# Kernel optimization log

Hardware: AMD Instinct MI355X
Metric: run time of the kernel (lower is better)

## Reference

```python
import jax, jax.numpy as jnp
import numpy as np

ITER_STEPS = 2


def setup_inputs() -> dict:
    key = jax.random.key(0)
    ks = jax.random.split(key, 9)
    B, N, D, E = 64, 256, 512, 10  # batch, nodes, node_dim, edge types
    node = jax.random.normal(ks[0], (B, N, D), dtype=jnp.float32)
    node_mask = jax.random.randint(ks[1], (B, N), 0, 2).astype(jnp.int32)
    adj = jax.random.randint(ks[2], (E, B, N, N), 0, 2).astype(jnp.int32)
    s = 0.02
    W_nw = jax.random.normal(ks[3], (1, D), dtype=jnp.float32) * s   # node weight fc [out=1, in=D]
    b_nw = jnp.zeros((1,), dtype=jnp.float32)
    W_self = jax.random.normal(ks[4], (D, D), dtype=jnp.float32) * s
    b_self = jnp.zeros((D,), dtype=jnp.float32)
    W_edge = jax.random.normal(ks[5], (E, D, D), dtype=jnp.float32) * s  # per-edge-type Linear (no bias)
    return {"node": node, "W_nw": W_nw, "b_nw": b_nw, "W_self": W_self,
            "b_self": b_self, "W_edge": W_edge, "node_mask": node_mask, "adj": adj}


def reference(node, W_nw, b_nw, W_self, b_self, W_edge, node_mask, adj):
    # node: [B,N,D]; node_mask: [B,N] int; adj: [E=10,B,N,N] int (binary)
    B, N, D = node.shape
    m = node_mask.astype(node.dtype)
    eye = jnp.eye(N, dtype=node.dtype)
    # dd_graph = mask outer-product with zeroed diagonal: [B,N,N]
    dd = m[:, None, :] * m[:, :, None] * (1.0 - eye)
    graphs = dd[None] * adj.astype(node.dtype)  # [E,B,N,N]
    # total neighbor count across all 10 edge types, clamped to >=1 (replace_masked_values)
    neigh = graphs.sum(axis=(0, 3))                       # [B,N]
    neigh = jnp.where(neigh >= 1.0, neigh, 1.0)
    all_weight = []
    for _ in range(ITER_STEPS):
        # (1) node relatedness gate
        w = jax.nn.sigmoid(node @ W_nw.T + b_nw)[..., 0]  # [B,N]
        all_weight.append(w)
        self_info = node @ W_self.T + b_self              # [B,N,D]
        # (2) per-edge-type projection + masked adjacency matmul, summed over edge types
        proj = jnp.einsum('bnk,edk->ebnd', node, W_edge)  # [E,B,N,D]
        masked_w = jnp.where(graphs != 0, w[None, :, None, :], 0.0)  # [E,B,N,N]
        agg = jnp.einsum('ebnm,ebmd->bnd', masked_w, proj)           # [B,N,D]
        # (3) update
        node = jax.nn.relu(self_info + agg / neigh[..., None])
    return node, jnp.stack(all_weight, axis=1)  # ([B,N,D], [B,ITER,N])
```

## Files before the change

kernel.cpp:

```cpp
#include <hip/hip_runtime.h>
#include <hip/hip_bf16.h>

#define BB 64
#define NN 256
#define DD 512
#define EE 10

typedef __bf16 bf16x8 __attribute__((ext_vector_type(8)));
typedef unsigned short ushort8v __attribute__((ext_vector_type(8)));
typedef unsigned int uint4v __attribute__((ext_vector_type(4)));
typedef unsigned int uint2v __attribute__((ext_vector_type(2)));
typedef float floatx4 __attribute__((ext_vector_type(4)));
typedef float floatx16 __attribute__((ext_vector_type(16)));

typedef __attribute__((address_space(3))) unsigned short lds_us;
typedef const __attribute__((address_space(1))) unsigned short glb_us;

__device__ __forceinline__ unsigned short f2b(float f) {
    union { float f; unsigned u; } x; x.f = f;
    unsigned r = x.u + 0x7FFFu + ((x.u >> 16) & 1u);
    return (unsigned short)(r >> 16);
}
__device__ __forceinline__ float b2f(unsigned short u) {
    union { unsigned u; float f; } x; x.u = ((unsigned)u) << 16;
    return x.f;
}
__device__ __forceinline__ unsigned pack_bf16(float a, float b) {
    union { float f; unsigned u; } xa, xb2; xa.f = a; xb2.f = b;
    return __builtin_amdgcn_perm(xa.u + 0x8000u, xb2.u + 0x8000u, 0x07060302u);
}

__global__ void k_wconv(const float* __restrict__ W_edge,
                        const float* __restrict__ W_self,
                        unsigned short* __restrict__ Wf) {
    int t = blockIdx.x * 256 + threadIdx.x;
    int lane  = t & 63;
    int kstep = (t >> 6) & 31;
    int cfg   = (t >> 11) & 15;
    int e     = t >> 15;
    int dout = cfg * 32 + (lane & 31);
    int k    = kstep * 16 + (lane >> 5) * 8;
    const float* src = (e < EE) ? (W_edge + ((size_t)e * DD + dout) * DD + k)
                                : (W_self + (size_t)dout * DD + k);
    ushort8v o;
    #pragma unroll
    for (int j = 0; j < 8; j++) o[j] = f2b(src[j]);
    *(ushort8v*)(Wf + (size_t)t * 8) = o;
}

__global__ void k_graph(const int* __restrict__ adj, const int* __restrict__ mask,
                        unsigned* __restrict__ packed, float* __restrict__ recip) {
    int b = blockIdx.x >> 8;
    int n = blockIdx.x & 255;
    int lane = threadIdx.x & 63;
    int wv   = threadIdx.x >> 6;
    int m = wv * 64 + lane;
    int ok = (mask[b * NN + n] != 0) & (mask[b * NN + m] != 0) & (m != n);
    __shared__ int cnt_s[4];
    int total = 0;
    #pragma unroll
    for (int e = 0; e < EE; e++) {
        int a = adj[(((size_t)e * BB + b) * NN + n) * NN + m];
        int bit = ok & (a != 0);
        unsigned long long bal = __ballot(bit);
        if (lane == 0) {
            unsigned* dst = packed + (((size_t)e * BB + b) * NN + n) * 8 + wv * 2;
            dst[0] = (unsigned)bal;
            dst[1] = (unsigned)(bal >> 32);
        }
        total += bit;
    }
    for (int off = 32; off; off >>= 1) total += __shfl_down(total, off);
    if (lane == 0) cnt_s[wv] = total;
    __syncthreads();
    if (threadIdx.x == 0) {
        int c = cnt_s[0] + cnt_s[1] + cnt_s[2] + cnt_s[3];
        recip[b * NN + n] = 1.0f / (float)(c < 1 ? 1 : c);
    }
}

template<int TI>
__global__ __launch_bounds__(256)
void k_gt(const float* __restrict__ xf, const unsigned short* __restrict__ xbin,
          const float* __restrict__ W_nw, const float* __restrict__ b_nw,
          float* __restrict__ w_out, unsigned short* __restrict__ wTf,
          unsigned short* __restrict__ xb0) {
    int bid = blockIdx.x;
    int b  = bid >> 4;
    int ms = bid & 15;
    __shared__ float part[16][17];
    __shared__ float wsig[16];
    int t = threadIdx.x;
    int row = t >> 4;
    int seg = t & 15;
    size_t g = ((size_t)(b * NN + ms * 16 + row)) * DD + seg * 32;
    float s = 0.f;
    if (TI == 0) {
        const floatx4* xp = (const floatx4*)(xf + g);
        const floatx4* wp = (const floatx4*)(W_nw + seg * 32);
        #pragma unroll
        for (int k = 0; k < 4; k++) {
            floatx4 a = xp[2 * k], c4 = xp[2 * k + 1];
            floatx4 wa = wp[2 * k], wc = wp[2 * k + 1];
            ushort8v u;
            #pragma unroll
            for (int j = 0; j < 4; j++) {
                s += a[j] * wa[j] + c4[j] * wc[j];
                u[j] = f2b(a[j]); u[4 + j] = f2b(c4[j]);
            }
            *(ushort8v*)(xb0 + g + k * 8) = u;
        }
    } else {
        const ushort8v* xp = (const ushort8v*)(xbin + g);
        const float* wp = W_nw + seg * 32;
        #pragma unroll
        for (int k = 0; k < 4; k++) {
            ushort8v u = xp[k];
            #pragma unroll
            for (int j = 0; j < 8; j++) s += b2f(u[j]) * wp[k * 8 + j];
        }
    }
    part[row][seg] = s;
    __syncthreads();
    if (t < 16) {
        float tot = 0.f;
        #pragma unroll
        for (int i = 0; i < 16; i++) tot += part[t][i];
        float v = 1.f / (1.f + __expf(-(tot + b_nw[0])));
        wsig[t] = v;
        w_out[(b * 2 + TI) * NN + ms * 16 + t] = v;
    }
    __syncthreads();
    #pragma unroll
    for (int c = 0; c < 4; c++) {
        int slot = t + 256 * c;
        int dd_  = slot >> 6;
        int lane = slot & 63;
        int l31 = lane & 31, hi = lane >> 5;
        size_t xrow = ((size_t)(b * NN + ms * 16 + hi * 8)) * DD + dd_ * 32 + l31;
        ushort8v o;
        #pragma unroll
        for (int j = 0; j < 8; j++) {
            float xv = (TI == 0) ? xf[xrow + (size_t)j * DD] : b2f(xbin[xrow + (size_t)j * DD]);
            o[j] = f2b(xv * wsig[hi * 8 + j]);
        }
        *(ushort8v*)(wTf + ((((size_t)b * 16 + ms) * 16 + dd_) * 64 + lane) * 8) = o;
    }
}

template<int TI>
__global__ __launch_bounds__(512, 2)
void k2_heavy(const unsigned short* __restrict__ wTf,
              const unsigned short* __restrict__ xb,
              const unsigned short* __restrict__ Wf,
              const unsigned* __restrict__ packed,
              const float* __restrict__ recip,
              const float* __restrict__ b_self,
              unsigned short* __restrict__ out_bf16,
              float* __restrict__ out_f32) {
    __shared__ __attribute__((aligned(16))) unsigned short sWT[2][32 * 512];
    __shared__ __attribute__((aligned(16))) unsigned short sTf[2][8 * 512];

    int bid = blockIdx.x;
    int b  = bid & 63;
    int nq = bid >> 6;
    int w = threadIdx.x >> 6, lane = threadIdx.x & 63;
    int l31 = lane & 31, hi = lane >> 5;

    int sd = w & 1, sn = (w >> 1) & 1;
    int gn1 = nq * 64 + sn * 32 + l31;
    float rn = recip[b * NN + gn1];

    floatx16 acc2[2][2];
    #pragma unroll
    for (int i = 0; i < 2; i++)
        #pragma unroll
        for (int jj = 0; jj < 2; jj++)
            #pragma unroll
            for (int q = 0; q < 16; q++) acc2[i][jj][q] = 0.f;

    auto stage_sWT = [&](int dc, int buf) {
        #pragma unroll
        for (int it = 0; it < 4; it++) {
            int c = it * 8 + w;
            const unsigned short* g = wTf +
                ((((size_t)b * 16 + (c >> 1)) * 16 + dc * 2 + (c & 1)) * 64 + lane) * 8;
            __builtin_amdgcn_global_load_lds((glb_us*)g, (lds_us*)&sWT[buf][c * 512], 16, 0, 0);
        }
    };

    stage_sWT(0, 0);

    bf16x8 Bg[16];
    const unsigned short* WfL = Wf + lane * 8;
    const unsigned short* xbL = xb + ((size_t)(b * NN + nq * 64 + l31)) * DD + hi * 8;

    #pragma unroll 1
    for (int s = 0; s < 89; s++) {
        int cur = s & 1;
        if (s <= 80) {
            asm volatile("s_waitcnt vmcnt(0) lgkmcnt(0)" ::: "memory");
            __builtin_amdgcn_s_barrier();
            if (s + 1 < 80) stage_sWT((s + 1) & 7, (s + 1) & 1);
        }
        if (s < 80 && w < 4) {
            int e = s >> 3;
            if ((s & 7) == 0) {
                const uint4v* pp = (const uint4v*)(packed +
                    (((size_t)e * BB + b) * NN + gn1) * 8);
                uint4v pa = pp[0], pb = pp[1];
                unsigned pw[8] = {pa[0], pa[1], pa[2], pa[3], pb[0], pb[1], pb[2], pb[3]};
                #pragma unroll
                for (int ks = 0; ks < 16; ks++) {
                    int byi = ks * 2 + hi;
                    unsigned byte_ = (pw[byi >> 2] >> ((byi & 3) * 8)) & 0xFFu;
                    uint4v av;
                    #pragma unroll
                    for (int p2 = 0; p2 < 4; p2++) {
                        unsigned tt = (byte_ >> (2 * p2)) & 3u;
                        unsigned u = (tt | (tt << 15)) & 0x10001u;
                        av[p2] = u * 0x3F80u;
                    }
                    Bg[ks] = __builtin_bit_cast(bf16x8, av);
                }
            }
            floatx16 acc3a, acc3b;
            #pragma unroll
            for (int q = 0; q < 16; q++) { acc3a[q] = 0.f; acc3b[q] = 0.f; }
            #pragma unroll
            for (int ks = 0; ks < 8; ks++) {
                bf16x8 afrA = __builtin_bit_cast(bf16x8,
                    *(const ushort8v*)&sWT[cur][((2 * ks) * 2 + sd) * 512 + lane * 8]);
                bf16x8 afrB = __builtin_bit_cast(bf16x8,
                    *(const ushort8v*)&sWT[cur][((2 * ks + 1) * 2 + sd) * 512 + lane * 8]);
                acc3a = __builtin_amdgcn_mfma_f32_32x32x16_bf16(afrA, Bg[2 * ks],     acc3a, 0, 0, 0);
                acc3b = __builtin_amdgcn_mfma_f32_32x32x16_bf16(afrB, Bg[2 * ks + 1], acc3b, 0, 0, 0);
            }
            #pragma unroll
            for (int g = 0; g < 4; g++) {
                float v0 = (acc3a[g * 4 + 0] + acc3b[g * 4 + 0]) * rn;
                float v1 = (acc3a[g * 4 + 1] + acc3b[g * 4 + 1]) * rn;
                float v2 = (acc3a[g * 4 + 2] + acc3b[g * 4 + 2]) * rn;
                float v3 = (acc3a[g * 4 + 3] + acc3b[g * 4 + 3]) * rn;
                uint2v pk;
                pk[0] = pack_bf16(v1, v0);
                pk[1] = pack_bf16(v3, v2);
                int kk = sd * 2 + (g >> 1);
                int slot = (kk * 2 + sn) * 64 + (g & 1) * 32 + l31;
                *(uint2v*)&sTf[cur][slot * 8 + 4 * hi] = pk;
            }
        }
        if (s >= 1) {
            int q = s - 1;
            int qe = q >> 3, qdc = q & 7, pb2 = q & 1;
            if (qe < EE) {
                const unsigned short* sTfL = &sTf[pb2][lane * 8];
                #pragma unroll
                for (int kk = 0; kk < 4; kk++) {
                    bf16x8 afr[2];
                    #pragma unroll
                    for (int nb = 0; nb < 2; nb++)
                        afr[nb] = __builtin_bit_cast(bf16x8,
                            *(const ushort8v*)&sTfL[(kk * 2 + nb) * 512]);
                    #pragma unroll
                    for (int cb = 0; cb < 2; cb++) {
                        bf16x8 bfr = __builtin_bit_cast(bf16x8, *(const ushort8v*)
                            &WfL[(size_t)(((qe * 16 + w * 2 + cb) * 32 + qdc * 4 + kk)) * 512]);
                        #pragma unroll
                        for (int nb = 0; nb < 2; nb++)
                            acc2[nb][cb] = __builtin_amdgcn_mfma_f32_32x32x16_bf16(
                                afr[nb], bfr, acc2[nb][cb], 0, 0, 0);
                    }
                }
            } else {
                #pragma unroll
                for (int kk = 0; kk < 4; kk++) {
                    bf16x8 afr[2];
                    #pragma unroll
                    for (int nb = 0; nb < 2; nb++)
                        afr[nb] = __builtin_bit_cast(bf16x8, *(const ushort8v*)
                            &xbL[(size_t)nb * 32 * DD + qdc * 64 + kk * 16]);
                    #pragma unroll
                    for (int cb = 0; cb < 2; cb++) {
                        bf16x8 bfr = __builtin_bit_cast(bf16x8, *(const ushort8v*)
                            &WfL[(size_t)(((EE * 16 + w * 2 + cb) * 32 + qdc * 4 + kk)) * 512]);
                        #pragma unroll
                        for (int nb = 0; nb < 2; nb++)
                            acc2[nb][cb] = __builtin_amdgcn_mfma_f32_32x32x16_bf16(
                                afr[nb], bfr, acc2[nb][cb], 0, 0, 0);
                    }
                }
            }
        }
    }
    #pragma unroll
    for (int cb = 0; cb < 2; cb++) {
        int col = w * 64 + cb * 32 + l31;
        float bs = b_self[col];
        #pragma unroll
        for (int nb = 0; nb < 2; nb++) {
            #pragma unroll
            for (int rg = 0; rg < 16; rg++) {
                int row = nq * 64 + nb * 32 + (rg & 3) + 8 * (rg >> 2) + 4 * hi;
                float v = acc2[nb][cb][rg] + bs;
                v = v > 0.f ? v : 0.f;
                size_t gi = ((size_t)b * NN + row) * DD + col;
                if (TI == 0) out_bf16[gi] = f2b(v);
                else         out_f32[gi] = v;
            }
        }
    }
}

extern "C" void kernel_launch(void* const* d_in, const int* in_sizes, int n_in,
                              void* d_out, int out_size, void* d_ws, size_t ws_size,
                              hipStream_t stream) {
    const float* node   = (const float*)d_in[0];
    const float* W_nw   = (const float*)d_in[1];
    const float* b_nw   = (const float*)d_in[2];
    const float* W_self = (const float*)d_in[3];
    const float* b_self = (const float*)d_in[4];
    const float* W_edge = (const float*)d_in[5];
    const int*   mask   = (const int*)d_in[6];
    const int*   adj    = (const int*)d_in[7];
    float* out = (float*)d_out;
    float* out_w = out + (size_t)BB * NN * DD;

    char* ws = (char*)d_ws;
    size_t off = 0;
    unsigned short* Wf    = (unsigned short*)(ws + off); off += (size_t)11 * DD * DD * 2;
    unsigned short* wTf   = (unsigned short*)(ws + off); off += (size_t)BB * DD * NN * 2;
    unsigned short* xb0   = (unsigned short*)(ws + off); off += (size_t)BB * NN * DD * 2;
    unsigned short* xb1   = (unsigned short*)(ws + off); off += (size_t)BB * NN * DD * 2;
    unsigned*       packed= (unsigned*)(ws + off);       off += (size_t)EE * BB * NN * 8 * 4;
    float*          recip = (float*)(ws + off);          off += (size_t)BB * NN * 4;

    k_wconv<<<dim3(1408), dim3(256), 0, stream>>>(W_edge, W_self, Wf);
    k_graph<<<dim3(16384), dim3(256), 0, stream>>>(adj, mask, packed, recip);

    k_gt<0><<<dim3(1024), dim3(256), 0, stream>>>(node, nullptr, W_nw, b_nw, out_w, wTf, xb0);
    k2_heavy<0><<<dim3(256), dim3(512), 0, stream>>>(wTf, xb0, Wf, packed, recip, b_self, xb1, nullptr);

    k_gt<1><<<dim3(1024), dim3(256), 0, stream>>>(nullptr, xb1, W_nw, b_nw, out_w, wTf, nullptr);
    k2_heavy<1><<<dim3(256), dim3(512), 0, stream>>>(wTf, xb1, Wf, packed, recip, b_self, nullptr, out);
}
```

Baseline: 748.8 us.

## Split output columns across two blocks to double grid and raise occupancy

```diff
diff --git a/kernel.cpp b/kernel.cpp
--- a/kernel.cpp
+++ b/kernel.cpp
@@ -149,7 +149,7 @@
 }
 
 template<int TI>
-__global__ __launch_bounds__(512, 2)
+__global__ __launch_bounds__(512, 4)
 void k2_heavy(const unsigned short* __restrict__ wTf,
               const unsigned short* __restrict__ xb,
               const unsigned short* __restrict__ Wf,
@@ -163,7 +163,8 @@
 
     int bid = blockIdx.x;
     int b  = bid & 63;
-    int nq = bid >> 6;
+    int nq = (bid >> 6) & 3;
+    int ct = bid >> 8;
     int w = threadIdx.x >> 6, lane = threadIdx.x & 63;
     int l31 = lane & 31, hi = lane >> 5;
 
@@ -171,27 +172,24 @@
     int gn1 = nq * 64 + sn * 32 + l31;
     float rn = recip[b * NN + gn1];
 
-    floatx16 acc2[2][2];
+    floatx16 acc2[2];
     #pragma unroll
     for (int i = 0; i < 2; i++)
         #pragma unroll
-        for (int jj = 0; jj < 2; jj++)
-            #pragma unroll
-            for (int q = 0; q < 16; q++) acc2[i][jj][q] = 0.f;
-
-    auto stage_sWT = [&](int dc, int buf) {
+        for (int q = 0; q < 16; q++) acc2[i][q] = 0.f;
+
+    auto stage_sWT = [&](int dcs, int buf) {
         #pragma unroll
         for (int it = 0; it < 4; it++) {
             int c = it * 8 + w;
             const unsigned short* g = wTf +
-                ((((size_t)b * 16 + (c >> 1)) * 16 + dc * 2 + (c & 1)) * 64 + lane) * 8;
+                ((((size_t)b * 16 + (c >> 1)) * 16 + dcs * 2 + (c & 1)) * 64 + lane) * 8;
             __builtin_amdgcn_global_load_lds((glb_us*)g, (lds_us*)&sWT[buf][c * 512], 16, 0, 0);
         }
     };
 
     stage_sWT(0, 0);
 
-    bf16x8 Bg[16];
     const unsigned short* WfL = Wf + lane * 8;
     const unsigned short* xbL = xb + ((size_t)(b * NN + nq * 64 + l31)) * DD + hi * 8;
 
@@ -205,25 +203,9 @@
         }
         if (s < 80 && w < 4) {
             int e = s >> 3;
-            if ((s & 7) == 0) {
-                const uint4v* pp = (const uint4v*)(packed +
-                    (((size_t)e * BB + b) * NN + gn1) * 8);
-                uint4v pa = pp[0], pb = pp[1];
-                unsigned pw[8] = {pa[0], pa[1], pa[2], pa[3], pb[0], pb[1], pb[2], pb[3]};
-                #pragma unroll
-                for (int ks = 0; ks < 16; ks++) {
-                    int byi = ks * 2 + hi;
-                    unsigned byte_ = (pw[byi >> 2] >> ((byi & 3) * 8)) & 0xFFu;
-                    uint4v av;
-                    #pragma unroll
-                    for (int p2 = 0; p2 < 4; p2++) {
-                        unsigned tt = (byte_ >> (2 * p2)) & 3u;
-                        unsigned u = (tt | (tt << 15)) & 0x10001u;
-                        av[p2] = u * 0x3F80u;
-                    }
-                    Bg[ks] = __builtin_bit_cast(bf16x8, av);
-                }
-            }
+            const uint4v* pp = (const uint4v*)(packed +
+                (((size_t)e * BB + b) * NN + gn1) * 8);
+            uint4v pa = pp[0], pbv = pp[1];
             floatx16 acc3a, acc3b;
             #pragma unroll
             for (int q = 0; q < 16; q++) { acc3a[q] = 0.f; acc3b[q] = 0.f; }
@@ -233,8 +215,22 @@
                     *(const ushort8v*)&sWT[cur][((2 * ks) * 2 + sd) * 512 + lane * 8]);
                 bf16x8 afrB = __builtin_bit_cast(bf16x8,
                     *(const ushort8v*)&sWT[cur][((2 * ks + 1) * 2 + sd) * 512 + lane * 8]);
-                acc3a = __builtin_amdgcn_mfma_f32_32x32x16_bf16(afrA, Bg[2 * ks],     acc3a, 0, 0, 0);
-                acc3b = __builtin_amdgcn_mfma_f32_32x32x16_bf16(afrB, Bg[2 * ks + 1], acc3b, 0, 0, 0);
+                bf16x8 bg[2];
+                #pragma unroll
+                for (int half = 0; half < 2; half++) {
+                    int ksx = 2 * ks + half;
+                    unsigned word = (ksx < 8) ? pa[ksx >> 1] : pbv[(ksx >> 1) - 4];
+                    unsigned byte_ = (word >> ((ksx & 1) * 16 + hi * 8)) & 0xFFu;
+                    uint4v av;
+                    #pragma unroll
+                    for (int p2 = 0; p2 < 4; p2++) {
+                        unsigned tt = (byte_ >> (2 * p2)) & 3u;
+                        av[p2] = ((tt | (tt << 15)) & 0x10001u) * 0x3F80u;
+                    }
+                    bg[half] = __builtin_bit_cast(bf16x8, av);
+                }
+                acc3a = __builtin_amdgcn_mfma_f32_32x32x16_bf16(afrA, bg[0], acc3a, 0, 0, 0);
+                acc3b = __builtin_amdgcn_mfma_f32_32x32x16_bf16(afrB, bg[1], acc3b, 0, 0, 0);
             }
             #pragma unroll
             for (int g = 0; g < 4; g++) {
@@ -257,52 +253,43 @@
                 const unsigned short* sTfL = &sTf[pb2][lane * 8];
                 #pragma unroll
                 for (int kk = 0; kk < 4; kk++) {
-                    bf16x8 afr[2];
-                    #pragma unroll
-                    for (int nb = 0; nb < 2; nb++)
-                        afr[nb] = __builtin_bit_cast(bf16x8,
-                            *(const ushort8v*)&sTfL[(kk * 2 + nb) * 512]);
-                    #pragma unroll
-                    for (int cb = 0; cb < 2; cb++) {
-                        bf16x8 bfr = __builtin_bit_cast(bf16x8, *(const ushort8v*)
-                            &WfL[(size_t)(((qe * 16 + w * 2 + cb) * 32 + qdc * 4 + kk)) * 512]);
-                        #pragma unroll
-                        for (int nb = 0; nb < 2; nb++)
-                            acc2[nb][cb] = __builtin_amdgcn_mfma_f32_32x32x16_bf16(
-                                afr[nb], bfr, acc2[nb][cb], 0, 0, 0);
-                    }
+                    bf16x8 afr0 = __builtin_bit_cast(bf16x8,
+                        *(const ushort8v*)&sTfL[(kk * 2 + 0) * 512]);
+                    bf16x8 afr1 = __builtin_bit_cast(bf16x8,
+                        *(const ushort8v*)&sTfL[(kk * 2 + 1) * 512]);
+                    bf16x8 bfr = __builtin_bit_cast(bf16x8, *(const ushort8v*)
+                        &WfL[(size_t)(((qe * 16 + ct * 8 + w) * 32 + qdc * 4 + kk)) * 512]);
+                    acc2[0] = __builtin_amdgcn_mfma_f32_32x32x16_bf16(
+                        afr0, bfr, acc2[0], 0, 0, 0);
+                    acc2[1] = __builtin_amdgcn_mfma_f32_32x32x16_bf16(
+                        afr1, bfr, acc2[1], 0, 0, 0);
                 }
             } else {
                 #pragma unroll
                 for (int kk = 0; kk < 4; kk++) {
-                    bf16x8 afr[2];
-                    #pragma unroll
-                    for (int nb = 0; nb < 2; nb++)
-                        afr[nb] = __builtin_bit_cast(bf16x8, *(const ushort8v*)
-                            &xbL[(size_t)nb * 32 * DD + qdc * 64 + kk * 16]);
-                    #pragma unroll
-                    for (int cb = 0; cb < 2; cb++) {
-                        bf16x8 bfr = __builtin_bit_cast(bf16x8, *(const ushort8v*)
-                            &WfL[(size_t)(((EE * 16 + w * 2 + cb) * 32 + qdc * 4 + kk)) * 512]);
-                        #pragma unroll
-                        for (int nb = 0; nb < 2; nb++)
-                            acc2[nb][cb] = __builtin_amdgcn_mfma_f32_32x32x16_bf16(
-                                afr[nb], bfr, acc2[nb][cb], 0, 0, 0);
-                    }
+                    bf16x8 afr0 = __builtin_bit_cast(bf16x8, *(const ushort8v*)
+                        &xbL[(size_t)0 * 32 * DD + qdc * 64 + kk * 16]);
+                    bf16x8 afr1 = __builtin_bit_cast(bf16x8, *(const ushort8v*)
+                        &xbL[(size_t)1 * 32 * DD + qdc * 64 + kk * 16]);
+                    bf16x8 bfr = __builtin_bit_cast(bf16x8, *(const ushort8v*)
+                        &WfL[(size_t)(((EE * 16 + ct * 8 + w) * 32 + qdc * 4 + kk)) * 512]);
+                    acc2[0] = __builtin_amdgcn_mfma_f32_32x32x16_bf16(
+                        afr0, bfr, acc2[0], 0, 0, 0);
+                    acc2[1] = __builtin_amdgcn_mfma_f32_32x32x16_bf16(
+                        afr1, bfr, acc2[1], 0, 0, 0);
                 }
             }
         }
     }
-    #pragma unroll
-    for (int cb = 0; cb < 2; cb++) {
-        int col = w * 64 + cb * 32 + l31;
+    {
+        int col = ct * 256 + w * 32 + l31;
         float bs = b_self[col];
         #pragma unroll
         for (int nb = 0; nb < 2; nb++) {
             #pragma unroll
             for (int rg = 0; rg < 16; rg++) {
                 int row = nq * 64 + nb * 32 + (rg & 3) + 8 * (rg >> 2) + 4 * hi;
-                float v = acc2[nb][cb][rg] + bs;
+                float v = acc2[nb][rg] + bs;
                 v = v > 0.f ? v : 0.f;
                 size_t gi = ((size_t)b * NN + row) * DD + col;
                 if (TI == 0) out_bf16[gi] = f2b(v);
@@ -339,8 +326,8 @@
     k_graph<<<dim3(16384), dim3(256), 0, stream>>>(adj, mask, packed, recip);
 
     k_gt<0><<<dim3(1024), dim3(256), 0, stream>>>(node, nullptr, W_nw, b_nw, out_w, wTf, xb0);
-    k2_heavy<0><<<dim3(256), dim3(512), 0, stream>>>(wTf, xb0, Wf, packed, recip, b_self, xb1, nullptr);
+    k2_heavy<0><<<dim3(512), dim3(512), 0, stream>>>(wTf, xb0, Wf, packed, recip, b_self, xb1, nullptr);
 
     k_gt<1><<<dim3(1024), dim3(256), 0, stream>>>(nullptr, xb1, W_nw, b_nw, out_w, wTf, nullptr);
-    k2_heavy<1><<<dim3(256), dim3(512), 0, stream>>>(wTf, xb1, Wf, packed, recip, b_self, nullptr, out);
-}
+    k2_heavy<1><<<dim3(512), dim3(512), 0, stream>>>(wTf, xb1, Wf, packed, recip, b_self, nullptr, out);
+}
```

After: 812.7 us. 8.5% more time.
